# Kernel optimization log

Hardware: AMD Instinct MI355X
Metric: run time of the kernel (lower is better)

The kernel has to match this reference:

```python
import jax, jax.numpy as jnp
import numpy as np

B, T, F, H = 2048, 256, 64, 128


def setup_inputs() -> dict:
    key = jax.random.key(0)
    ks = jax.random.split(key, 9)
    s = 0.1  # small init scale for stable recurrence
    return {
        "x": jax.random.normal(ks[0], (B, T, F), dtype=jnp.float32),
        "W_ih": jax.random.normal(ks[1], (4 * H, F), dtype=jnp.float32) * s,
        "W_hh": jax.random.normal(ks[2], (4 * H, H), dtype=jnp.float32) * s,
        "b_ih": jax.random.normal(ks[3], (4 * H,), dtype=jnp.float32) * s,
        "b_hh": jax.random.normal(ks[4], (4 * H,), dtype=jnp.float32) * s,
        "W1": jax.random.normal(ks[5], (32, H), dtype=jnp.float32) * s,
        "b1": jax.random.normal(ks[6], (32,), dtype=jnp.float32) * s,
        "W2": jax.random.normal(ks[7], (1, 32), dtype=jnp.float32) * s,
        "b2": jax.random.normal(ks[8], (1,), dtype=jnp.float32) * s,
    }


def reference(x, W_ih, W_hh, b_ih, b_hh, W1, b1, W2, b2):
    # Single-layer LSTM (PyTorch gate order i, f, g, o), take last hidden state.
    Bsz, Tlen, _ = x.shape
    Hdim = W_hh.shape[1]
    xt = jnp.swapaxes(x, 0, 1)  # [T, B, F]
    bias = b_ih + b_hh  # [4H]

    def step(carry, xb):
        h, c = carry
        gates = xb @ W_ih.T + h @ W_hh.T + bias  # [B, 4H]
        i, f, g, o = jnp.split(gates, 4, axis=-1)
        i = jax.nn.sigmoid(i)
        f = jax.nn.sigmoid(f)
        g = jnp.tanh(g)
        o = jax.nn.sigmoid(o)
        c = f * c + i * g
        h = o * jnp.tanh(c)
        return (h, c), None

    h0 = jnp.zeros((Bsz, Hdim), dtype=x.dtype)
    c0 = jnp.zeros((Bsz, Hdim), dtype=x.dtype)
    (h_last, _), _ = jax.lax.scan(step, (h0, c0), xt)

    # head: Linear(H,32) -> ReLU -> Linear(32,1) -> Sigmoid -> squeeze(-1)
    z = jax.nn.relu(h_last @ W1.T + b1)
    return jax.nn.sigmoid(z @ W2.T + b2)[:, 0]
```

## Files before the change

### kernel.cpp

```cpp
#include <hip/hip_runtime.h>


#define Bsz   2048
#define Tlen  256
#define Fdim  64
#define Hdim  128
#define ROWS  8
#define NTH   512
#define TILE_E 512
#define NKT   6
#define BUF_E (NKT * TILE_E)

using bf16x8 = __attribute__((ext_vector_type(8))) __bf16;
using f32x4  = __attribute__((ext_vector_type(4))) float;

__device__ __forceinline__ float fast_rcp(float x) {
#if __has_builtin(__builtin_amdgcn_rcpf)
    return __builtin_amdgcn_rcpf(x);
#else
    return 1.0f / x;
#endif
}
__device__ __forceinline__ float fast_exp2(float x) {
#if __has_builtin(__builtin_amdgcn_exp2f)
    return __builtin_amdgcn_exp2f(x);
#else
    return exp2f(x);
#endif
}
#define LOG2E  1.4426950408889634f
#define LOG2E2 2.8853900817779268f

__device__ __forceinline__ bf16x8 cvt8(float4 a, float4 b) {
    bf16x8 r;
    r[0]=(__bf16)a.x; r[1]=(__bf16)a.y; r[2]=(__bf16)a.z; r[3]=(__bf16)a.w;
    r[4]=(__bf16)b.x; r[5]=(__bf16)b.y; r[6]=(__bf16)b.z; r[7]=(__bf16)b.w;
    return r;
}

__device__ __forceinline__ int frag_elem(int row, int k) {
    return (k >> 5) * TILE_E + ((((k >> 3) & 3) * 16 + row) * 8) + (k & 7);
}

__global__ __launch_bounds__(NTH, 2)
void lstm_fused(const float* __restrict__ x,
                const float* __restrict__ W_ih,
                const float* __restrict__ W_hh,
                const float* __restrict__ b_ih,
                const float* __restrict__ b_hh,
                const float* __restrict__ W1,
                const float* __restrict__ b1,
                const float* __restrict__ W2,
                const float* __restrict__ b2,
                float* __restrict__ out)
{
    __shared__ __bf16 Abuf[2][BUF_E];
    __shared__ float  hlast[ROWS * Hdim];
    __shared__ float  zbuf[ROWS * 32];

    const int tid  = threadIdx.x;
    const int w    = tid >> 6;
    const int lane = tid & 63;
    const int quad = lane >> 4;
    const int l16  = lane & 15;
    const int b0   = blockIdx.x * ROWS;
    const bool hiq = (quad >= 2);

    bf16x8 bwx[2][4], bwh[4][4];
    #pragma unroll
    for (int kt = 0; kt < NKT; ++kt) {
        const int k0 = kt * 32 + quad * 8;
        #pragma unroll
        for (int g = 0; g < 4; ++g) {
            const int n = g * Hdim + w * 16 + l16;
            const float* p = (kt < 2) ? (W_ih + (size_t)n * Fdim + k0)
                                      : (W_hh + (size_t)n * Hdim + (k0 - Fdim));
            float4 lo = *(const float4*)p;
            float4 hi = *(const float4*)(p + 4);
            bf16x8 r = cvt8(lo, hi);
            if (kt < 2) bwx[kt][g] = r; else bwh[kt - 2][g] = r;
        }
    }
    f32x4 biasf[4];
    #pragma unroll
    for (int g = 0; g < 4; ++g) {
        const int n = g * Hdim + w * 16 + l16;
        const float bv = b_ih[n] + b_hh[n];
        biasf[g] = (f32x4){bv, bv, bv, bv};
    }

    const bool sx_on  = tid < 256;
    const int  sx_row = tid & 7;
    const int  sx_fp  = (tid >> 3) & 31;
    const int  f0     = 2 * sx_fp;
    const float* xrp  = x + (size_t)(b0 + sx_row) * (Tlen * Fdim) + f0;
    const int sx_e0 = frag_elem(sx_row,     f0);
    const int sx_e1 = frag_elem(sx_row + 8, f0);

    const int r0  = (quad >> 1) * 2;
    const int brb = (quad & 1) * 4 + r0;
    const int hc  = 16 * w + l16;
    const int h_e0a = frag_elem(brb,         Fdim + hc);
    const int h_e0b = frag_elem(brb + 8,     Fdim + hc);
    const int h_e1a = frag_elem(brb + 1,     Fdim + hc);
    const int h_e1b = frag_elem(brb + 1 + 8, Fdim + hc);

    #pragma unroll
    for (int i = 0; i < BUF_E / NTH; ++i)
        Abuf[0][tid + i * NTH] = (__bf16)0.0f;
    __syncthreads();
    float2 xpA = make_float2(0.f, 0.f);
    float2 xpB = make_float2(0.f, 0.f);
    if (sx_on) {
        float2 v1 = *(const float2*)(xrp + Fdim);
        __bf16 a1[2] = {(__bf16)v1.x, (__bf16)v1.y};
        *(uint*)&Abuf[0][sx_e0] = *(uint*)a1;
        *(uint*)&Abuf[0][sx_e1] = *(uint*)a1;
        xpA = *(const float2*)(xrp + 2 * Fdim);
        xpB = *(const float2*)(xrp + 3 * Fdim);
    }
    f32x4 xacc[4];
    {
        const float* x0p = x + (size_t)(b0 + (l16 & 7)) * (Tlen * Fdim) + quad * 8;
        float4 a0 = *(const float4*)(x0p);
        float4 a1 = *(const float4*)(x0p + 4);
        float4 a2 = *(const float4*)(x0p + 32);
        float4 a3 = *(const float4*)(x0p + 36);
        bf16x8 xi0 = cvt8(a0, a1), xi1 = cvt8(a2, a3);
        #pragma unroll
        for (int g = 0; g < 4; ++g) {
            f32x4 tmp = __builtin_amdgcn_mfma_f32_16x16x32_bf16(xi0, bwx[0][g], biasf[g], 0, 0, 0);
            xacc[g]   = __builtin_amdgcn_mfma_f32_16x16x32_bf16(xi1, bwx[1][g], tmp, 0, 0, 0);
        }
    }
    __syncthreads();

    float cc0 = 0.0f, cc1 = 0.0f;

    auto step = [&](int t, const __bf16* __restrict__ rb,
                    __bf16* __restrict__ wbf, float2& xstage) {
        bf16x8 hf[4];
        #pragma unroll
        for (int kt = 0; kt < 4; ++kt)
            hf[kt] = *(const bf16x8*)&rb[(2 + kt) * TILE_E + lane * 8];
        bf16x8 xf0 = *(const bf16x8*)&rb[lane * 8];
        bf16x8 xf1 = *(const bf16x8*)&rb[TILE_E + lane * 8];

        float2 xcur = xstage;
        if (sx_on && (t + 4) < Tlen)
            xstage = *(const float2*)(xrp + (size_t)(t + 4) * Fdim);

        f32x4 acc[4];
        #pragma unroll
        for (int g = 0; g < 4; ++g)
            acc[g] = __builtin_amdgcn_mfma_f32_16x16x32_bf16(hf[0], bwh[0][g], xacc[g], 0, 0, 0);
        #pragma unroll
        for (int kt = 1; kt < 4; ++kt) {
            #pragma unroll
            for (int g = 0; g < 4; ++g)
                acc[g] = __builtin_amdgcn_mfma_f32_16x16x32_bf16(hf[kt], bwh[kt][g], acc[g], 0, 0, 0);
        }

        if ((t + 1) < Tlen) {
            #pragma unroll
            for (int g = 0; g < 4; ++g) {
                f32x4 tmp = __builtin_amdgcn_mfma_f32_16x16x32_bf16(xf0, bwx[0][g], biasf[g], 0, 0, 0);
                xacc[g]   = __builtin_amdgcn_mfma_f32_16x16x32_bf16(xf1, bwx[1][g], tmp, 0, 0, 0);
            }
        }

        if (sx_on && (t + 2) < Tlen) {
            __bf16 xa[2] = {(__bf16)xcur.x, (__bf16)xcur.y};
            *(uint*)&wbf[sx_e0] = *(uint*)xa;
            *(uint*)&wbf[sx_e1] = *(uint*)xa;
        }

        __builtin_amdgcn_sched_barrier(0);

        {
            float gi = hiq ? acc[0][2] : acc[0][0];
            float gf = hiq ? acc[1][2] : acc[1][0];
            float gg = hiq ? acc[2][2] : acc[2][0];
            float go = hiq ? acc[3][2] : acc[3][0];
            float ei = fast_exp2(-LOG2E  * gi);
            float ef = fast_exp2(-LOG2E  * gf);
            float eg = fast_exp2(-LOG2E2 * gg);
            float eo = fast_exp2(-LOG2E  * go);
            float a = 1.0f + ef, b = 1.0f + ei, d = 1.0f + eg;
            float bd  = b * d;
            float num = cc0 * bd + a * (1.0f - eg);
            cc0 = num * fast_rcp(a * bd);
            float ec = fast_exp2(-LOG2E2 * cc0);
            float h  = (1.0f - ec) * fast_rcp((1.0f + eo) * (1.0f + ec));
            __bf16 hb = (__bf16)h;
            wbf[h_e0a] = hb;
            wbf[h_e0b] = hb;
            if (t == Tlen - 1) hlast[brb * Hdim + hc] = h;
        }
        {
            float gi = hiq ? acc[0][3] : acc[0][1];
            float gf = hiq ? acc[1][3] : acc[1][1];
            float gg = hiq ? acc[2][3] : acc[2][1];
            float go = hiq ? acc[3][3] : acc[3][1];
            float ei = fast_exp2(-LOG2E  * gi);
            float ef = fast_exp2(-LOG2E  * gf);
            float eg = fast_exp2(-LOG2E2 * gg);
            float eo = fast_exp2(-LOG2E  * go);
            float a = 1.0f + ef, b = 1.0f + ei, d = 1.0f + eg;
            float bd  = b * d;
            float num = cc1 * bd + a * (1.0f - eg);
            cc1 = num * fast_rcp(a * bd);
            float ec = fast_exp2(-LOG2E2 * cc1);
            float h  = (1.0f - ec) * fast_rcp((1.0f + eo) * (1.0f + ec));
            __bf16 hb = (__bf16)h;
            wbf[h_e1a] = hb;
            wbf[h_e1b] = hb;
            if (t == Tlen - 1) hlast[(brb + 1) * Hdim + hc] = h;
        }

        asm volatile("s_waitcnt lgkmcnt(0)" ::: "memory");
        __builtin_amdgcn_s_barrier();
        __builtin_amdgcn_sched_barrier(0);
    };

    for (int t = 0; t < Tlen; t += 2) {
        step(t,     Abuf[0], Abuf[1], xpA);
        step(t + 1, Abuf[1], Abuf[0], xpB);
    }

    if (tid < ROWS * 32) {
        const int b = tid >> 5, n = tid & 31;
        const float4* w4 = (const float4*)(W1 + n * Hdim);
        const float4* h4 = (const float4*)(hlast + b * Hdim);
        float s = b1[n];
        #pragma unroll
        for (int kk = 0; kk < Hdim / 4; ++kk) {
            float4 wv = w4[kk];
            float4 hv = h4[kk];
            s += wv.x * hv.x + wv.y * hv.y + wv.z * hv.z + wv.w * hv.w;
        }
        zbuf[b * 32 + n] = fmaxf(s, 0.0f);
    }
    __syncthreads();
    if (tid < ROWS) {
        float s = b2[0];
        #pragma unroll
        for (int n = 0; n < 32; ++n) s += zbuf[tid * 32 + n] * W2[n];
        float e = fast_exp2(-LOG2E * s);
        out[b0 + tid] = fast_rcp(1.0f + e);
    }
}

extern "C" void kernel_launch(void* const* d_in, const int* in_sizes, int n_in,
                              void* d_out, int out_size, void* d_ws, size_t ws_size,
                              hipStream_t stream) {
    const float* x    = (const float*)d_in[0];
    const float* W_ih = (const float*)d_in[1];
    const float* W_hh = (const float*)d_in[2];
    const float* b_ih = (const float*)d_in[3];
    const float* b_hh = (const float*)d_in[4];
    const float* W1   = (const float*)d_in[5];
    const float* b1   = (const float*)d_in[6];
    const float* W2   = (const float*)d_in[7];
    const float* b2   = (const float*)d_in[8];
    float* out = (float*)d_out;

    dim3 grid(Bsz / ROWS), block(NTH);
    lstm_fused<<<grid, block, 0, stream>>>(x, W_ih, W_hh, b_ih, b_hh, W1, b1, W2, b2, out);
}
```

Baseline: 342.9 us.

## Split recurrent step into two wave-group windows overlapping cell math with MFMA

Each timestep is split into two barrier windows. Waves 0-3 own hidden columns 0-63 and waves 4-7 own columns 64-127. In window A, every wave finishes the gate MFMAs using the upper half of h, and the low waves run the cell update. In window B, every wave starts the next step's MFMAs on the freshly written lower half of h while the high waves run their cell update. The x-staging loads are moved to the high waves to balance work. The aim is to shorten the serial MFMA-to-activation chain per step, at the cost of twice as many block barriers and each wave group sitting idle for half the activation work.

```diff
diff --git a/kernel.cpp b/kernel.cpp
--- a/kernel.cpp
+++ b/kernel.cpp
@@ -64,7 +64,8 @@
     const int quad = lane >> 4;
     const int l16  = lane & 15;
     const int b0   = blockIdx.x * ROWS;
-    const bool hiq = (quad >= 2);
+    const bool hiq  = (quad >= 2);
+    const bool loW  = (w < 4);
 
     bf16x8 bwx[2][4], bwh[4][4];
     #pragma unroll
@@ -89,10 +90,10 @@
         biasf[g] = (f32x4){bv, bv, bv, bv};
     }
 
-    const bool sx_on  = tid < 256;
-    const int  sx_row = tid & 7;
-    const int  sx_fp  = (tid >> 3) & 31;
-    const int  f0     = 2 * sx_fp;
+    const bool sx_on  = tid >= 256;
+    const int  tix    = tid & 255;
+    const int  sx_row = tix & 7;
+    const int  f0     = 2 * ((tix >> 3) & 31);
     const float* xrp  = x + (size_t)(b0 + sx_row) * (Tlen * Fdim) + f0;
     const int sx_e0 = frag_elem(sx_row,     f0);
     const int sx_e1 = frag_elem(sx_row + 8, f0);
@@ -119,7 +120,7 @@
         xpA = *(const float2*)(xrp + 2 * Fdim);
         xpB = *(const float2*)(xrp + 3 * Fdim);
     }
-    f32x4 xacc[4];
+    f32x4 pacc[4];
     {
         const float* x0p = x + (size_t)(b0 + (l16 & 7)) * (Tlen * Fdim) + quad * 8;
         float4 a0 = *(const float4*)(x0p);
@@ -130,53 +131,16 @@
         #pragma unroll
         for (int g = 0; g < 4; ++g) {
             f32x4 tmp = __builtin_amdgcn_mfma_f32_16x16x32_bf16(xi0, bwx[0][g], biasf[g], 0, 0, 0);
-            xacc[g]   = __builtin_amdgcn_mfma_f32_16x16x32_bf16(xi1, bwx[1][g], tmp, 0, 0, 0);
+            pacc[g]   = __builtin_amdgcn_mfma_f32_16x16x32_bf16(xi1, bwx[1][g], tmp, 0, 0, 0);
         }
     }
     __syncthreads();
 
     float cc0 = 0.0f, cc1 = 0.0f;
-
-    auto step = [&](int t, const __bf16* __restrict__ rb,
-                    __bf16* __restrict__ wbf, float2& xstage) {
-        bf16x8 hf[4];
-        #pragma unroll
-        for (int kt = 0; kt < 4; ++kt)
-            hf[kt] = *(const bf16x8*)&rb[(2 + kt) * TILE_E + lane * 8];
-        bf16x8 xf0 = *(const bf16x8*)&rb[lane * 8];
-        bf16x8 xf1 = *(const bf16x8*)&rb[TILE_E + lane * 8];
-
-        float2 xcur = xstage;
-        if (sx_on && (t + 4) < Tlen)
-            xstage = *(const float2*)(xrp + (size_t)(t + 4) * Fdim);
-
-        f32x4 acc[4];
-        #pragma unroll
-        for (int g = 0; g < 4; ++g)
-            acc[g] = __builtin_amdgcn_mfma_f32_16x16x32_bf16(hf[0], bwh[0][g], xacc[g], 0, 0, 0);
-        #pragma unroll
-        for (int kt = 1; kt < 4; ++kt) {
-            #pragma unroll
-            for (int g = 0; g < 4; ++g)
-                acc[g] = __builtin_amdgcn_mfma_f32_16x16x32_bf16(hf[kt], bwh[kt][g], acc[g], 0, 0, 0);
-        }
-
-        if ((t + 1) < Tlen) {
-            #pragma unroll
-            for (int g = 0; g < 4; ++g) {
-                f32x4 tmp = __builtin_amdgcn_mfma_f32_16x16x32_bf16(xf0, bwx[0][g], biasf[g], 0, 0, 0);
-                xacc[g]   = __builtin_amdgcn_mfma_f32_16x16x32_bf16(xf1, bwx[1][g], tmp, 0, 0, 0);
-            }
-        }
-
-        if (sx_on && (t + 2) < Tlen) {
-            __bf16 xa[2] = {(__bf16)xcur.x, (__bf16)xcur.y};
-            *(uint*)&wbf[sx_e0] = *(uint*)xa;
-            *(uint*)&wbf[sx_e1] = *(uint*)xa;
-        }
-
-        __builtin_amdgcn_sched_barrier(0);
-
+    f32x4 acc[4];
+    f32x4 xaccN[4];
+
+    auto cellmath = [&](int t, __bf16* __restrict__ wbf) {
         {
             float gi = hiq ? acc[0][2] : acc[0][0];
             float gf = hiq ? acc[1][2] : acc[1][0];
@@ -217,15 +181,72 @@
             wbf[h_e1b] = hb;
             if (t == Tlen - 1) hlast[(brb + 1) * Hdim + hc] = h;
         }
+    };
+
+    auto windowA = [&](int t, const __bf16* __restrict__ rb,
+                       __bf16* __restrict__ wbf, float2& xstage) {
+        bf16x8 hf2 = *(const bf16x8*)&rb[(2 + 2) * TILE_E + lane * 8];
+        bf16x8 hf3 = *(const bf16x8*)&rb[(2 + 3) * TILE_E + lane * 8];
+        bf16x8 xf0 = *(const bf16x8*)&rb[lane * 8];
+        bf16x8 xf1 = *(const bf16x8*)&rb[TILE_E + lane * 8];
+
+        float2 xcur = xstage;
+        if (sx_on && (t + 4) < Tlen)
+            xstage = *(const float2*)(xrp + (size_t)(t + 4) * Fdim);
+
+        #pragma unroll
+        for (int g = 0; g < 4; ++g)
+            acc[g] = __builtin_amdgcn_mfma_f32_16x16x32_bf16(hf2, bwh[2][g], pacc[g], 0, 0, 0);
+        #pragma unroll
+        for (int g = 0; g < 4; ++g)
+            acc[g] = __builtin_amdgcn_mfma_f32_16x16x32_bf16(hf3, bwh[3][g], acc[g], 0, 0, 0);
+
+        if ((t + 1) < Tlen) {
+            #pragma unroll
+            for (int g = 0; g < 4; ++g) {
+                f32x4 tmp = __builtin_amdgcn_mfma_f32_16x16x32_bf16(xf0, bwx[0][g], biasf[g], 0, 0, 0);
+                xaccN[g]  = __builtin_amdgcn_mfma_f32_16x16x32_bf16(xf1, bwx[1][g], tmp, 0, 0, 0);
+            }
+        }
+
+        if (sx_on && (t + 2) < Tlen) {
+            __bf16 xa[2] = {(__bf16)xcur.x, (__bf16)xcur.y};
+            *(uint*)&wbf[sx_e0] = *(uint*)xa;
+            *(uint*)&wbf[sx_e1] = *(uint*)xa;
+        }
+
+        __builtin_amdgcn_sched_barrier(0);
+        if (loW) cellmath(t, wbf);
 
         asm volatile("s_waitcnt lgkmcnt(0)" ::: "memory");
         __builtin_amdgcn_s_barrier();
         __builtin_amdgcn_sched_barrier(0);
     };
 
+    auto windowB = [&](int t, __bf16* __restrict__ wbf) {
+        if ((t + 1) < Tlen) {
+            bf16x8 hf0 = *(const bf16x8*)&wbf[(2 + 0) * TILE_E + lane * 8];
+            bf16x8 hf1 = *(const bf16x8*)&wbf[(2 + 1) * TILE_E + lane * 8];
+            #pragma unroll
+            for (int g = 0; g < 4; ++g) {
+                f32x4 tmp = __builtin_amdgcn_mfma_f32_16x16x32_bf16(hf0, bwh[0][g], xaccN[g], 0, 0, 0);
+                pacc[g]   = __builtin_amdgcn_mfma_f32_16x16x32_bf16(hf1, bwh[1][g], tmp, 0, 0, 0);
+            }
+        }
+
+        __builtin_amdgcn_sched_barrier(0);
+        if (!loW) cellmath(t, wbf);
+
+        asm volatile("s_waitcnt lgkmcnt(0)" ::: "memory");
+        __builtin_amdgcn_s_barrier();
+        __builtin_amdgcn_sched_barrier(0);
+    };
+
     for (int t = 0; t < Tlen; t += 2) {
-        step(t,     Abuf[0], Abuf[1], xpA);
-        step(t + 1, Abuf[1], Abuf[0], xpB);
+        windowA(t,     Abuf[0], Abuf[1], xpA);
+        windowB(t,     Abuf[1]);
+        windowA(t + 1, Abuf[1], Abuf[0], xpB);
+        windowB(t + 1, Abuf[0]);
     }
 
     if (tid < ROWS * 32) {
```

Result: slower. 398.1 us (+16.1%).
